# Kernel optimization log

Hardware: AMD Instinct MI355X
Metric: run time of the kernel (lower is better)

## Reference

```python
import jax, jax.numpy as jnp
import numpy as np

D_THRE = 0.03  # spatial-consistency distance threshold from forward call
N_POINTS = 32768


def _pairwise_dist(x):
    """x: [M, 3] -> [M, M] Euclidean distance matrix, safe-sqrt (zero diag)."""
    diff = x[:, None, :] - x[None, :, :]          # [M, M, 3]
    sq = jnp.sum(diff * diff, axis=-1)            # [M, M]
    safe = jnp.where(sq > 0, sq, 1.0)
    return jnp.where(sq > 0, jnp.sqrt(safe), 0.0)


def setup_inputs() -> dict:
    key = jax.random.key(0)
    k1, k2 = jax.random.split(key)
    num_clusters = 64
    cluster_size = N_POINTS // num_clusters
    # LiDAR-scale point cloud (meters)
    pc1 = jax.random.normal(k1, (1, N_POINTS, 3), dtype=jnp.float32) * 20.0
    flow = jax.random.normal(k2, (1, N_POINTS, 3), dtype=jnp.float32) * 0.1
    # DBSCAN labels are constants computed at __init__; model them as
    # contiguous equal-size clusters so the ragged loop is jit-friendly.
    labels = jnp.arange(N_POINTS, dtype=jnp.int32) // cluster_size
    return {"flow": flow, "pc1": pc1, "labels": labels, "num_clusters": num_clusters}


def reference(flow, pc1, labels, num_clusters):
    n = pc1.shape[1]
    m = n // num_clusters  # points per cluster (labels are contiguous blocks)
    pc1_deformed = pc1 + flow
    src = pc1[0].reshape(num_clusters, m, 3)           # cluster gather == reshape
    tgt = pc1_deformed[0].reshape(num_clusters, m, 3)

    def cluster_sc_loss(s, t):
        # spatial_consistency_loss (SC2-PCR measure) for one cluster
        src_dist = _pairwise_dist(s)                   # [M, M]
        tgt_dist = _pairwise_dist(t)                   # [M, M]
        cross = jnp.abs(src_dist - tgt_dist)
        sc_measure = jnp.clip(1.0 - (cross * cross) / (D_THRE * D_THRE), 0.0)
        return jnp.mean(1.0 - sc_measure)

    losses = jax.vmap(cluster_sc_loss)(src, tgt)       # [K]
    loss_sc = jnp.sum(losses) / num_clusters
    return loss_sc
```

## Files before the change

### kernel.cpp

```cpp
#include <hip/hip_runtime.h>

#define M 512
#define K 64
#define CHUNKS 8
#define ROWS (M / CHUNKS)
#define NT 256

__global__ __launch_bounds__(NT) void sc_partial_kernel(
    const float* __restrict__ flow,
    const float* __restrict__ pc1,
    float* __restrict__ partial)
{
    __shared__ float sx[M], sy[M], sz[M];
    __shared__ float tx[M], ty[M], tz[M];
    __shared__ float wsum[NT / 64];

    const int blk = blockIdx.x;
    const int c   = blk / CHUNKS;
    const int rc  = blk % CHUNKS;
    const int tid = threadIdx.x;
    const int base = c * M * 3;

    for (int idx = tid; idx < M * 3; idx += NT) {
        float p = pc1[base + idx];
        float f = flow[base + idx];
        float t = p + f;
        int pt   = idx / 3;
        int comp = idx - pt * 3;
        if (comp == 0)      { sx[pt] = p; tx[pt] = t; }
        else if (comp == 1) { sy[pt] = p; ty[pt] = t; }
        else                { sz[pt] = p; tz[pt] = t; }
    }
    __syncthreads();

    const float inv_d2 = 1.0f / (0.03f * 0.03f);

    const float c0sx = sx[tid],      c0sy = sy[tid],      c0sz = sz[tid];
    const float c0tx = tx[tid],      c0ty = ty[tid],      c0tz = tz[tid];
    const float c1sx = sx[tid + NT], c1sy = sy[tid + NT], c1sz = sz[tid + NT];
    const float c1tx = tx[tid + NT], c1ty = ty[tid + NT], c1tz = tz[tid + NT];

    float acc = 0.0f;
    const int row0 = rc * ROWS;

#pragma unroll 4
    for (int r = 0; r < ROWS; ++r) {
        const int i = row0 + r;
        const float rsx = sx[i], rsy = sy[i], rsz = sz[i];
        const float rtx = tx[i], rty = ty[i], rtz = tz[i];

        {
            float dx = rsx - c0sx, dy = rsy - c0sy, dz = rsz - c0sz;
            float ds = sqrtf(dx * dx + dy * dy + dz * dz);
            float ex = rtx - c0tx, ey = rty - c0ty, ez = rtz - c0tz;
            float dt = sqrtf(ex * ex + ey * ey + ez * ez);
            float diff = ds - dt;
            acc += fminf(diff * diff * inv_d2, 1.0f);
        }
        {
            float dx = rsx - c1sx, dy = rsy - c1sy, dz = rsz - c1sz;
            float ds = sqrtf(dx * dx + dy * dy + dz * dz);
            float ex = rtx - c1tx, ey = rty - c1ty, ez = rtz - c1tz;
            float dt = sqrtf(ex * ex + ey * ey + ez * ez);
            float diff = ds - dt;
            acc += fminf(diff * diff * inv_d2, 1.0f);
        }
    }

    for (int off = 32; off > 0; off >>= 1)
        acc += __shfl_down(acc, off, 64);
    const int lane = tid & 63;
    const int wave = tid >> 6;
    if (lane == 0) wsum[wave] = acc;
    __syncthreads();
    if (tid == 0) {
        float s = 0.0f;
        for (int w = 0; w < NT / 64; ++w) s += wsum[w];
        partial[blk] = s;
    }
}

__global__ __launch_bounds__(NT) void sc_reduce_kernel(
    const float* __restrict__ partial,
    float* __restrict__ out)
{
    __shared__ float wsum[NT / 64];
    const int tid = threadIdx.x;
    float v = partial[tid] + partial[tid + NT];
    for (int off = 32; off > 0; off >>= 1)
        v += __shfl_down(v, off, 64);
    const int lane = tid & 63;
    const int wave = tid >> 6;
    if (lane == 0) wsum[wave] = v;
    __syncthreads();
    if (tid == 0) {
        float s = 0.0f;
        for (int w = 0; w < NT / 64; ++w) s += wsum[w];
        out[0] = s * (1.0f / (float)((long long)M * M * K));
    }
}

extern "C" void kernel_launch(void* const* d_in, const int* in_sizes, int n_in,
                              void* d_out, int out_size, void* d_ws, size_t ws_size,
                              hipStream_t stream)
{
    const float* flow = (const float*)d_in[0];
    const float* pc1  = (const float*)d_in[1];
    float* partial = (float*)d_ws;
    float* out     = (float*)d_out;

    sc_partial_kernel<<<K * CHUNKS, NT, 0, stream>>>(flow, pc1, partial);
    sc_reduce_kernel<<<1, NT, 0, stream>>>(partial, out);
}
```

Measured before the change: 83.50 us.

## Exploit distance-matrix symmetry with 64x64 tiles, skip lower-triangle tiles

The kernel now splits each cluster's 512x512 pair matrix into an 8x8 grid of 64x64 tiles. Blocks whose tile lies below the diagonal exit early, and off-diagonal tiles are counted twice, which roughly halves the sqrt and pair arithmetic. It also switches to the raw hardware sqrt builtin and uses SoA shared tiles. In exchange the grid is much larger with many empty blocks, each block does far less work, and the final reduction has to sum 4096 partials.

```diff
diff --git a/kernel.cpp b/kernel.cpp
--- a/kernel.cpp
+++ b/kernel.cpp
@@ -2,81 +2,79 @@
 
 #define M 512
 #define K 64
-#define CHUNKS 8
-#define ROWS (M / CHUNKS)
+#define TP 64
+#define NTILE (M / TP)
 #define NT 256
 
-__global__ __launch_bounds__(NT) void sc_partial_kernel(
+__global__ __launch_bounds__(NT) void sc_tile_kernel(
     const float* __restrict__ flow,
     const float* __restrict__ pc1,
     float* __restrict__ partial)
 {
-    __shared__ float sx[M], sy[M], sz[M];
-    __shared__ float tx[M], ty[M], tz[M];
+    __shared__ float A[6][TP];
+    __shared__ float B[6][TP];
     __shared__ float wsum[NT / 64];
 
     const int blk = blockIdx.x;
-    const int c   = blk / CHUNKS;
-    const int rc  = blk % CHUNKS;
+    const int c   = blk >> 6;
+    const int tp  = blk & 63;
+    const int a   = tp >> 3;
+    const int b   = tp & 7;
     const int tid = threadIdx.x;
-    const int base = c * M * 3;
 
-    for (int idx = tid; idx < M * 3; idx += NT) {
-        float p = pc1[base + idx];
-        float f = flow[base + idx];
-        float t = p + f;
-        int pt   = idx / 3;
-        int comp = idx - pt * 3;
-        if (comp == 0)      { sx[pt] = p; tx[pt] = t; }
-        else if (comp == 1) { sy[pt] = p; ty[pt] = t; }
-        else                { sz[pt] = p; tz[pt] = t; }
+    if (a > b) {
+        if (tid == 0) partial[blk] = 0.0f;
+        return;
+    }
+
+    const int basea = (c * M + a * TP) * 3;
+    const int baseb = (c * M + b * TP) * 3;
+
+    for (int idx = tid; idx < 2 * 3 * TP; idx += NT) {
+        const int chunk = idx / (3 * TP);
+        const int e     = idx - chunk * (3 * TP);
+        const int gbase = chunk ? baseb : basea;
+        const float p = pc1[gbase + e];
+        const float f = flow[gbase + e];
+        const int pt = e / 3;
+        const int comp = e - pt * 3;
+        float* dst = chunk ? &B[0][0] : &A[0][0];
+        dst[comp * TP + pt]       = p;
+        dst[(comp + 3) * TP + pt] = p + f;
     }
     __syncthreads();
 
     const float inv_d2 = 1.0f / (0.03f * 0.03f);
+    const int lane = tid & 63;
+    const int wave = tid >> 6;
 
-    const float c0sx = sx[tid],      c0sy = sy[tid],      c0sz = sz[tid];
-    const float c0tx = tx[tid],      c0ty = ty[tid],      c0tz = tz[tid];
-    const float c1sx = sx[tid + NT], c1sy = sy[tid + NT], c1sz = sz[tid + NT];
-    const float c1tx = tx[tid + NT], c1ty = ty[tid + NT], c1tz = tz[tid + NT];
+    const float csx = B[0][lane], csy = B[1][lane], csz = B[2][lane];
+    const float ctx = B[3][lane], cty = B[4][lane], ctz = B[5][lane];
 
     float acc = 0.0f;
-    const int row0 = rc * ROWS;
+    const int r0 = wave * (TP / 4);
 
-#pragma unroll 4
-    for (int r = 0; r < ROWS; ++r) {
-        const int i = row0 + r;
-        const float rsx = sx[i], rsy = sy[i], rsz = sz[i];
-        const float rtx = tx[i], rty = ty[i], rtz = tz[i];
+#pragma unroll
+    for (int rr = 0; rr < TP / 4; ++rr) {
+        const int r = r0 + rr;
+        const float rsx = A[0][r], rsy = A[1][r], rsz = A[2][r];
+        const float rtx = A[3][r], rty = A[4][r], rtz = A[5][r];
 
-        {
-            float dx = rsx - c0sx, dy = rsy - c0sy, dz = rsz - c0sz;
-            float ds = sqrtf(dx * dx + dy * dy + dz * dz);
-            float ex = rtx - c0tx, ey = rty - c0ty, ez = rtz - c0tz;
-            float dt = sqrtf(ex * ex + ey * ey + ez * ez);
-            float diff = ds - dt;
-            acc += fminf(diff * diff * inv_d2, 1.0f);
-        }
-        {
-            float dx = rsx - c1sx, dy = rsy - c1sy, dz = rsz - c1sz;
-            float ds = sqrtf(dx * dx + dy * dy + dz * dz);
-            float ex = rtx - c1tx, ey = rty - c1ty, ez = rtz - c1tz;
-            float dt = sqrtf(ex * ex + ey * ey + ez * ez);
-            float diff = ds - dt;
-            acc += fminf(diff * diff * inv_d2, 1.0f);
-        }
+        const float dx = rsx - csx, dy = rsy - csy, dz = rsz - csz;
+        const float ds = __builtin_amdgcn_sqrtf(dx * dx + dy * dy + dz * dz);
+        const float ex = rtx - ctx, ey = rty - cty, ez = rtz - ctz;
+        const float dt = __builtin_amdgcn_sqrtf(ex * ex + ey * ey + ez * ez);
+        const float d = ds - dt;
+        acc += fminf(d * d * inv_d2, 1.0f);
     }
 
     for (int off = 32; off > 0; off >>= 1)
         acc += __shfl_down(acc, off, 64);
-    const int lane = tid & 63;
-    const int wave = tid >> 6;
     if (lane == 0) wsum[wave] = acc;
     __syncthreads();
     if (tid == 0) {
-        float s = 0.0f;
-        for (int w = 0; w < NT / 64; ++w) s += wsum[w];
-        partial[blk] = s;
+        float s = wsum[0] + wsum[1] + wsum[2] + wsum[3];
+        partial[blk] = (a == b) ? s : 2.0f * s;
     }
 }
 
@@ -86,7 +84,8 @@
 {
     __shared__ float wsum[NT / 64];
     const int tid = threadIdx.x;
-    float v = partial[tid] + partial[tid + NT];
+    float v = 0.0f;
+    for (int i = tid; i < K * 64; i += NT) v += partial[i];
     for (int off = 32; off > 0; off >>= 1)
         v += __shfl_down(v, off, 64);
     const int lane = tid & 63;
@@ -109,6 +108,6 @@
     float* partial = (float*)d_ws;
     float* out     = (float*)d_out;
 
-    sc_partial_kernel<<<K * CHUNKS, NT, 0, stream>>>(flow, pc1, partial);
+    sc_tile_kernel<<<K * 64, NT, 0, stream>>>(flow, pc1, partial);
     sc_reduce_kernel<<<1, NT, 0, stream>>>(partial, out);
 }
```

Result: faster. 73.60 us (-11.8%).
